# Optimization experiments

Measured on AMD Instinct MI355X. Metric: run time of the kernel, lower is better.

Reference implementation:

```python
import jax, jax.numpy as jnp
import numpy as np

N_NODES = 100000
N_EDGES = 3200000
N_GRAPHS = 1024

def _lin(x, W, b):
    return x @ W.T + b

def _gine(x, src, dst, edge_attr, W, b, n_nodes):
    # message = relu(x_j + e); aggregate sum at dst; out = Linear(x + aggr)  (eps=0)
    msg = jax.nn.relu(x[src] + edge_attr)
    aggr = jax.ops.segment_sum(msg, dst, num_segments=n_nodes)
    return _lin(x + aggr, W, b)

def setup_inputs() -> dict:
    key = jax.random.key(0)
    ks = jax.random.split(key, 20)
    D_NODE, D_EDGE, H, OUT = 12, 4, 15, 2
    inp = {
        "x": jax.random.normal(ks[0], (N_NODES, D_NODE), dtype=jnp.float32),
        "edge_index": jax.random.randint(ks[1], (2, N_EDGES), 0, N_NODES, dtype=jnp.int64),
        "edge_attr": jax.random.normal(ks[2], (N_EDGES, D_EDGE), dtype=jnp.float32),
        "batch": jnp.sort(jax.random.randint(ks[3], (N_NODES,), 0, N_GRAPHS, dtype=jnp.int64)),
        # edge converters
        "Wec1": jax.random.normal(ks[4], (D_NODE, D_EDGE), dtype=jnp.float32) * 0.3,
        "bec1": jnp.zeros((D_NODE,), jnp.float32),
        "Wec2": jax.random.normal(ks[5], (H, D_NODE), dtype=jnp.float32) * 0.2,
        "bec2": jnp.zeros((H,), jnp.float32),
        # GINE layer linears
        "Wl0": jax.random.normal(ks[6], (H, D_NODE), dtype=jnp.float32) * 0.2,
        "bl0": jnp.zeros((H,), jnp.float32),
        "Wl1": jax.random.normal(ks[7], (H, H), dtype=jnp.float32) * 0.2,
        "bl1": jnp.zeros((H,), jnp.float32),
        "Wl2": jax.random.normal(ks[8], (H, H), dtype=jnp.float32) * 0.2,
        "bl2": jnp.zeros((H,), jnp.float32),
        # output head
        "Wo1": jax.random.normal(ks[9], (H, H), dtype=jnp.float32) * 0.2,
        "bo1": jnp.zeros((H,), jnp.float32),
        "Wo2": jax.random.normal(ks[10], (OUT, H), dtype=jnp.float32) * 0.2,
        "bo2": jnp.zeros((OUT,), jnp.float32),
    }
    return inp

def reference(x, edge_index, edge_attr, batch,
              Wec1, bec1, Wec2, bec2,
              Wl0, bl0, Wl1, bl1, Wl2, bl2,
              Wo1, bo1, Wo2, bo2):
    src, dst = edge_index[0], edge_index[1]
    n = x.shape[0]
    ea = _lin(edge_attr, Wec1, bec1)                 # [E, 12]
    h = jax.nn.elu(_gine(x, src, dst, ea, Wl0, bl0, n))   # [N, 15]
    ea2 = _lin(ea, Wec2, bec2)                       # [E, 15]
    h = jax.nn.elu(_gine(h, src, dst, ea2, Wl1, bl1, n))
    h = jax.nn.elu(_gine(h, src, dst, ea2, Wl2, bl2, n))
    pooled = jax.ops.segment_sum(h, batch, num_segments=N_GRAPHS)  # [G, 15]
    out = _lin(pooled, Wo1, bo1)
    # dropout(p=0.1) is identity in eval mode
    out = _lin(out, Wo2, bo2)                        # [G, 2]
    return out
```

## Files before the change

kernel.cpp:

```cpp
#include <hip/hip_runtime.h>
#include <hip/hip_fp16.h>
#include <math.h>

#define D_NODE 12
#define HS     16
#define BSH    7
#define BSZ    128
#define CHUNK  8192
#define HALF   4096
#define MAXNB  1024

__device__ __forceinline__ int wave_iscan(int v, int lane) {
#pragma unroll
    for (int d = 1; d < 64; d <<= 1) {
        int u = __shfl_up(v, d, 64);
        if (lane >= d) v += u;
    }
    return v;
}

__device__ __forceinline__ uint2 pack4(float4 a) {
    __half2 lo = __floats2half2_rn(a.x, a.y);
    __half2 hi = __floats2half2_rn(a.z, a.w);
    uint2 r;
    r.x = *reinterpret_cast<unsigned*>(&lo);
    r.y = *reinterpret_cast<unsigned*>(&hi);
    return r;
}

__device__ __forceinline__ float4 unpack4(uint2 u) {
    __half2 lo = *reinterpret_cast<__half2*>(&u.x);
    __half2 hi = *reinterpret_cast<__half2*>(&u.y);
    float2 f0 = __half22float2(lo), f1 = __half22float2(hi);
    return make_float4(f0.x, f0.y, f1.x, f1.y);
}

__global__ __launch_bounds__(256) void k_xcvt(
    const float* __restrict__ x, long long nn, __half* __restrict__ xp)
{
    long long idx = (long long)blockIdx.x * 256 + threadIdx.x;
    if (idx >= nn * HS) return;
    long long n = idx >> 4;
    int l = (int)(idx & 15);
    xp[idx] = __float2half_rn((l < D_NODE) ? x[n * D_NODE + l] : 0.f);
}

__global__ __launch_bounds__(1024) void k_p1(
    const int* __restrict__ ei, long long ne, int NB, int* __restrict__ M)
{
    __shared__ int cnt[MAXNB];
    int t = threadIdx.x;
    for (int k = t; k < NB; k += 1024) cnt[k] = 0;
    __syncthreads();
    long long beg = (long long)blockIdx.x * CHUNK;
    long long end = beg + CHUNK; if (end > ne) end = ne;
    for (long long e = beg + t; e < end; e += 1024)
        atomicAdd(&cnt[ei[ne + e] >> BSH], 1);
    __syncthreads();
    int* row = M + (long long)blockIdx.x * NB;
    for (int k = t; k < NB; k += 1024) row[k] = cnt[k];
}

__global__ __launch_bounds__(256) void k_colscan(
    int* __restrict__ M, int nblk, int NB, int* __restrict__ tot)
{
    __shared__ int wsum[4];
    int k = blockIdx.x;
    int t = threadIdx.x;
    int lane = t & 63, wv = t >> 6;
    int v[4]; int s = 0;
#pragma unroll
    for (int j = 0; j < 4; ++j) {
        int b = t * 4 + j;
        v[j] = (b < nblk) ? M[(long long)b * NB + k] : 0;
        s += v[j];
    }
    int inc = wave_iscan(s, lane);
    if (lane == 63) wsum[wv] = inc;
    __syncthreads();
    int base = inc - s;
#pragma unroll
    for (int j = 0; j < 4; ++j) { if (j < wv) base += wsum[j]; }
#pragma unroll
    for (int j = 0; j < 4; ++j) {
        int b = t * 4 + j;
        if (b < nblk) { M[(long long)b * NB + k] = base; base += v[j]; }
    }
    if (t == 255) tot[k] = base;
}

__global__ __launch_bounds__(1024) void k_bb(
    const int* __restrict__ tot, int NB, int* __restrict__ bb)
{
    __shared__ int wsum[16];
    int t = threadIdx.x;
    int lane = t & 63, wv = t >> 6;
    int c = (t < NB) ? tot[t] : 0;
    int inc = wave_iscan(c, lane);
    if (lane == 63) wsum[wv] = inc;
    __syncthreads();
    if (t < 16) {
        int s2 = wsum[t];
#pragma unroll
        for (int d = 1; d < 16; d <<= 1) {
            int u = __shfl_up(s2, d, 64);
            if (t >= d) s2 += u;
        }
        wsum[t] = s2;
    }
    __syncthreads();
    int base = (wv == 0) ? 0 : wsum[wv - 1];
    int incl = base + inc;
    if (t < NB) bb[t] = incl - c;
    if (t == NB - 1) bb[NB] = incl;
}

__global__ __launch_bounds__(1024) void k_p2(
    const int* __restrict__ ei, long long ne, const float4* __restrict__ attr,
    const int* __restrict__ M, const int* __restrict__ bb, int NB,
    unsigned* __restrict__ sp1, uint2* __restrict__ sattr1)
{
    __shared__ int lcnt[MAXNB];
    __shared__ int excl[MAXNB];
    __shared__ int gb[MAXNB];
    __shared__ int wsum[16];
    __shared__ unsigned sp_st[HALF];
    __shared__ uint2   sat_st[HALF];
    __shared__ int     gd_st[HALF];
    int t = threadIdx.x;
    int lane = t & 63, wv = t >> 6;
    const int* row = M + (long long)blockIdx.x * NB;
    gb[t]   = (t < NB) ? (bb[t] + row[t]) : 0;
    lcnt[t] = 0;
    __syncthreads();
    long long beg = (long long)blockIdx.x * CHUNK;
    long long end = beg + CHUNK; if (end > ne) end = ne;
    int nloc = (int)(end - beg);
    unsigned pk8[8]; uint2 a8[8]; int k8[8], r8[8];
#pragma unroll
    for (int j = 0; j < 8; ++j) {
        long long e = beg + t + (long long)j * 1024;
        if (e < end) {
            int s = ei[e];
            int d = ei[ne + e];
            a8[j] = pack4(attr[e]);
            int k = d >> BSH;
            k8[j] = k;
            pk8[j] = (unsigned)s | ((unsigned)(d & (BSZ - 1)) << 20);
            r8[j] = atomicAdd(&lcnt[k], 1);
        } else k8[j] = -1;
    }
    __syncthreads();
    int c = lcnt[t];
    int inc = wave_iscan(c, lane);
    if (lane == 63) wsum[wv] = inc;
    __syncthreads();
    if (t < 16) {
        int s2 = wsum[t];
#pragma unroll
        for (int d = 1; d < 16; d <<= 1) {
            int u = __shfl_up(s2, d, 64);
            if (t >= d) s2 += u;
        }
        wsum[t] = s2;
    }
    __syncthreads();
    excl[t] = inc - c + ((wv == 0) ? 0 : wsum[wv - 1]);
    __syncthreads();
    int idx8[8];
#pragma unroll
    for (int j = 0; j < 8; ++j)
        idx8[j] = (k8[j] >= 0) ? (excl[k8[j]] + r8[j]) : -1;
#pragma unroll
    for (int q = 0; q < 2; ++q) {
        int lo = q * HALF;
#pragma unroll
        for (int j = 0; j < 8; ++j) {
            int idx = idx8[j] - lo;
            if (idx8[j] >= 0 && idx >= 0 && idx < HALF) {
                sp_st[idx]  = pk8[j];
                sat_st[idx] = a8[j];
                gd_st[idx]  = gb[k8[j]] + r8[j];
            }
        }
        __syncthreads();
        for (int p = t; p < HALF; p += 1024) {
            int gp = lo + p;
            if (gp < nloc) {
                int gd = gd_st[p];
                sp1[gd]    = sp_st[p];
                sattr1[gd] = sat_st[p];
            }
        }
        __syncthreads();
    }
}

__global__ __launch_bounds__(1024) void k_p3(
    const unsigned* __restrict__ sp1, const uint2* __restrict__ sattr1,
    const int* __restrict__ bb, int NB, long long nn,
    unsigned* __restrict__ sp2, uint2* __restrict__ sattr2, int* __restrict__ off)
{
    __shared__ int cnt[BSZ];
    __shared__ int stage[BSZ];
    __shared__ int wsum0;
    int k = blockIdx.x, t = threadIdx.x;
    int lane = t & 63, wv = t >> 6;
    int beg = bb[k], end = bb[k + 1];
    if (t < BSZ) cnt[t] = 0;
    __syncthreads();
    for (int e = beg + t; e < end; e += 1024)
        atomicAdd(&cnt[sp1[e] >> 20], 1);
    __syncthreads();
    if (t < BSZ) {
        int c = cnt[t];
        int inc = wave_iscan(c, lane);
        stage[t] = inc;
        if (lane == 63 && wv == 0) wsum0 = inc;
    }
    __syncthreads();
    if (t < BSZ) {
        int c = cnt[t];
        int incl = stage[t] + ((wv == 1) ? wsum0 : 0);
        int excl = beg + incl - c;
        long long n = (long long)k * BSZ + t;
        if (n < nn) off[n] = excl;
        cnt[t] = excl;
    }
    if (k == NB - 1 && t == 0) off[nn] = end;
    __syncthreads();
    for (int e = beg + t; e < end; e += 1024) {
        unsigned pk = sp1[e];
        int ld = pk >> 20;
        int p = atomicAdd(&cnt[ld], 1);
        sp2[p] = pk & 0xFFFFF;
        sattr2[p] = sattr1[e];
    }
}

__global__ __launch_bounds__(256) void k_layer0(
    const __half* __restrict__ xp, long long nn, const int* __restrict__ off,
    const unsigned* __restrict__ sp2, const uint2* __restrict__ sattr2,
    const float* __restrict__ Wec1, const float* __restrict__ bec1,
    const float* __restrict__ Wl, const float* __restrict__ bl,
    __half* __restrict__ hout)
{
    __shared__ float sW1[64], sb1[16], sWl[16 * 17], sbl[16];
    int t = threadIdx.x;
    if (t < 64)  sW1[t] = (t < 48) ? Wec1[t] : 0.f;
    if (t < 16)  sb1[t] = (t < 12) ? bec1[t] : 0.f;
    { int i = t >> 4, j = t & 15;
      sWl[i * 17 + j] = (i < 15 && j < 12) ? Wl[i * 12 + j] : 0.f; }
    if (t < 16)  sbl[t] = (t < 15) ? bl[t] : 0.f;
    __syncthreads();
    int g = t >> 4, l = t & 15;
    long long n = (long long)blockIdx.x * 16 + g;
    if (n >= nn) return;
    int beg = off[n], end = off[n + 1];
    float w0 = sW1[l*4+0], w1 = sW1[l*4+1], w2 = sW1[l*4+2], w3 = sW1[l*4+3];
    float b1 = sb1[l];
    float xn = __half2float(xp[(n << 4) + l]);
    float acc = 0.f;
#pragma unroll 8
    for (int e = beg; e < end; ++e) {
        unsigned s = sp2[e];
        float4 a = unpack4(sattr2[e]);
        float xs = __half2float(xp[((long long)s << 4) + l]);
        float ea = b1 + w0 * a.x + w1 * a.y + w2 * a.z + w3 * a.w;
        acc += fmaxf(xs + ea, 0.f);
    }
    float v = xn + acc;
    float r = sbl[l];
#pragma unroll
    for (int j = 0; j < 12; ++j) {
        float vj = __shfl(v, j, 16);
        r += vj * sWl[l * 17 + j];
    }
    float o = r > 0.f ? r : expm1f(r);
    hout[(n << 4) + l] = __float2half_rn((l < 15) ? o : 0.f);
}

template<bool POOL, bool STORE>
__global__ __launch_bounds__(256) void k_layerK(
    const __half* __restrict__ h, long long nn, const int* __restrict__ off,
    const unsigned* __restrict__ sp2, const uint2* __restrict__ sattr2,
    const float* __restrict__ Wec1, const float* __restrict__ bec1,
    const float* __restrict__ Wec2, const float* __restrict__ bec2,
    const float* __restrict__ Wl, const float* __restrict__ bl,
    __half* __restrict__ hout, const int* __restrict__ batch, float* __restrict__ pooled)
{
    __shared__ float sW12[64], sb12[16], sWl[16 * 17], sbl[16];
    int t = threadIdx.x;
    if (t < 64) {
        int i = t >> 2, kk = t & 3;
        float a = 0.f;
        if (i < 15) {
#pragma unroll
            for (int j = 0; j < 12; ++j) a += Wec2[i*12+j] * Wec1[j*4+kk];
        }
        sW12[t] = a;
    }
    if (t < 16) {
        float a = 0.f;
        if (t < 15) {
            a = bec2[t];
#pragma unroll
            for (int j = 0; j < 12; ++j) a += Wec2[t*12+j] * bec1[j];
        }
        sb12[t] = a;
    }
    { int i = t >> 4, j = t & 15;
      sWl[i * 17 + j] = (i < 15 && j < 15) ? Wl[i * 15 + j] : 0.f; }
    if (t < 16) sbl[t] = (t < 15) ? bl[t] : 0.f;
    __syncthreads();
    int g = t >> 4, l = t & 15;
    long long n = (long long)blockIdx.x * 16 + g;
    if (n >= nn) return;
    int beg = off[n], end = off[n + 1];
    float w0 = sW12[l*4+0], w1 = sW12[l*4+1], w2 = sW12[l*4+2], w3 = sW12[l*4+3];
    float b12 = sb12[l];
    float hn = __half2float(h[(n << 4) + l]);
    float acc = 0.f;
#pragma unroll 8
    for (int e = beg; e < end; ++e) {
        unsigned s = sp2[e];
        float4 a = unpack4(sattr2[e]);
        float hs = __half2float(h[((long long)s << 4) + l]);
        float e2 = b12 + w0 * a.x + w1 * a.y + w2 * a.z + w3 * a.w;
        acc += fmaxf(hs + e2, 0.f);
    }
    float v = hn + acc;
    float r = sbl[l];
#pragma unroll
    for (int j = 0; j < 15; ++j) {
        float vj = __shfl(v, j, 16);
        r += vj * sWl[l * 17 + j];
    }
    float o = r > 0.f ? r : expm1f(r);
    if (STORE) hout[(n << 4) + l] = __float2half_rn((l < 15) ? o : 0.f);
    if (POOL && l < 15) atomicAdd(&pooled[(long long)batch[n] * HS + l], o);
}

__global__ __launch_bounds__(256) void k_head(
    const float* __restrict__ pooled, long long ng,
    const float* __restrict__ Wo1, const float* __restrict__ bo1,
    const float* __restrict__ Wo2, const float* __restrict__ bo2,
    float* __restrict__ out)
{
    long long g = (long long)blockIdx.x * 256 + threadIdx.x;
    if (g >= ng) return;
    float p[15], m[15];
#pragma unroll
    for (int j = 0; j < 15; ++j) p[j] = pooled[g * HS + j];
#pragma unroll
    for (int i = 0; i < 15; ++i) {
        float acc = bo1[i];
#pragma unroll
        for (int j = 0; j < 15; ++j) acc += p[j] * Wo1[i * 15 + j];
        m[i] = acc;
    }
#pragma unroll
    for (int i = 0; i < 2; ++i) {
        float acc = bo2[i];
#pragma unroll
        for (int j = 0; j < 15; ++j) acc += m[j] * Wo2[i * 15 + j];
        out[g * 2 + i] = acc;
    }
}

extern "C" void kernel_launch(void* const* d_in, const int* in_sizes, int n_in,
                              void* d_out, int out_size, void* d_ws, size_t ws_size,
                              hipStream_t stream)
{
    const float* x    = (const float*)d_in[0];
    const int*   ei   = (const int*)d_in[1];
    const float* attr = (const float*)d_in[2];
    const int*   batch= (const int*)d_in[3];
    const float* Wec1 = (const float*)d_in[4];
    const float* bec1 = (const float*)d_in[5];
    const float* Wec2 = (const float*)d_in[6];
    const float* bec2 = (const float*)d_in[7];
    const float* Wl0  = (const float*)d_in[8];
    const float* bl0  = (const float*)d_in[9];
    const float* Wl1  = (const float*)d_in[10];
    const float* bl1  = (const float*)d_in[11];
    const float* Wl2  = (const float*)d_in[12];
    const float* bl2  = (const float*)d_in[13];
    const float* Wo1  = (const float*)d_in[14];
    const float* bo1  = (const float*)d_in[15];
    const float* Wo2  = (const float*)d_in[16];
    const float* bo2  = (const float*)d_in[17];

    const long long nn = in_sizes[0] / D_NODE;
    const long long ne = in_sizes[1] / 2;
    const long long ng = out_size / 2;

    const int NB   = (int)((nn + BSZ - 1) >> BSH);
    const int nblk = (int)((ne + CHUNK - 1) / CHUNK);

    char* w = (char*)d_ws;
    uint2*    sattr1 = (uint2*)w;                 w += (size_t)ne * sizeof(uint2);
    unsigned* sp1    = (unsigned*)w;              w += (size_t)ne * sizeof(unsigned);
    uint2*    sattr2 = (uint2*)w;                 w += (size_t)ne * sizeof(uint2);
    unsigned* sp2    = (unsigned*)w;              w += (size_t)ne * sizeof(unsigned);
    int*      M      = (int*)w;                   w += (size_t)nblk * NB * sizeof(int);
    int*      tot    = (int*)w;                   w += (size_t)NB * sizeof(int);
    int*      bb     = (int*)w;                   w += ((size_t)NB + 1) * sizeof(int);
    int*      off    = (int*)w;                   w += ((size_t)nn + 1) * sizeof(int);
    w = (char*)(((uintptr_t)w + 15) & ~(uintptr_t)15);
    __half*   xp     = (__half*)w;                w += (size_t)nn * HS * sizeof(__half);
    __half*   hA     = (__half*)sattr1;
    __half*   hB     = hA + (size_t)nn * HS;
    float*    pooled = (float*)(hB + (size_t)nn * HS);
    float*    out    = (float*)d_out;

    k_xcvt<<<(int)((nn * HS + 255) / 256), 256, 0, stream>>>(x, nn, xp);

    k_p1<<<nblk, 1024, 0, stream>>>(ei, ne, NB, M);
    k_colscan<<<NB, 256, 0, stream>>>(M, nblk, NB, tot);
    k_bb<<<1, 1024, 0, stream>>>(tot, NB, bb);
    k_p2<<<nblk, 1024, 0, stream>>>(ei, ne, (const float4*)attr, M, bb, NB, sp1, sattr1);
    k_p3<<<NB, 1024, 0, stream>>>(sp1, sattr1, bb, NB, nn, sp2, sattr2, off);

    const int lblk = (int)((nn + 15) / 16);
    k_layer0<<<lblk, 256, 0, stream>>>(xp, nn, off, sp2, sattr2, Wec1, bec1, Wl0, bl0, hA);
    k_layerK<false, true><<<lblk, 256, 0, stream>>>(hA, nn, off, sp2, sattr2,
        Wec1, bec1, Wec2, bec2, Wl1, bl1, hB, nullptr, nullptr);
    hipMemsetAsync(pooled, 0, (size_t)ng * HS * sizeof(float), stream);
    k_layerK<true, false><<<lblk, 256, 0, stream>>>(hB, nn, off, sp2, sattr2,
        Wec1, bec1, Wec2, bec2, Wl2, bl2, nullptr, batch, pooled);

    k_head<<<(int)((ng + 255) / 256), 256, 0, stream>>>(pooled, ng, Wo1, bo1, Wo2, bo2, out);
}
```

Baseline: 264.2 us.

## Split each node's edge loop across four 16-lane slots per wavefront

The GINE layer kernels now give each node a whole 64-lane wavefront instead of a 16-lane group. The four 16-lane slots process interleaved edges and combine their partial sums with xor shuffles. The goal is more memory-level parallelism per node and shorter serial gather loops, in exchange for four times more blocks and idle lanes on low-degree nodes. Edge arrays are padded so reads past the end stay in bounds, and source indices are masked to 20 bits.

Measured after the change: 324.8 us. 1.23x slower.

```diff
diff --git a/kernel.cpp b/kernel.cpp
--- a/kernel.cpp
+++ b/kernel.cpp
@@ -28,9 +28,9 @@
     return r;
 }
 
-__device__ __forceinline__ float4 unpack4(uint2 u) {
-    __half2 lo = *reinterpret_cast<__half2*>(&u.x);
-    __half2 hi = *reinterpret_cast<__half2*>(&u.y);
+__device__ __forceinline__ float4 unpack4(unsigned ux, unsigned uy) {
+    __half2 lo = *reinterpret_cast<__half2*>(&ux);
+    __half2 hi = *reinterpret_cast<__half2*>(&uy);
     float2 f0 = __half22float2(lo), f1 = __half22float2(hi);
     return make_float4(f0.x, f0.y, f1.x, f1.y);
 }
@@ -253,22 +253,30 @@
       sWl[i * 17 + j] = (i < 15 && j < 12) ? Wl[i * 12 + j] : 0.f; }
     if (t < 16)  sbl[t] = (t < 15) ? bl[t] : 0.f;
     __syncthreads();
-    int g = t >> 4, l = t & 15;
-    long long n = (long long)blockIdx.x * 16 + g;
+    int wv = t >> 6;
+    int lane = t & 63;
+    int l = lane & 15;
+    int slot = lane >> 4;
+    long long n = (long long)blockIdx.x * 4 + wv;
     if (n >= nn) return;
     int beg = off[n], end = off[n + 1];
     float w0 = sW1[l*4+0], w1 = sW1[l*4+1], w2 = sW1[l*4+2], w3 = sW1[l*4+3];
     float b1 = sb1[l];
     float xn = __half2float(xp[(n << 4) + l]);
     float acc = 0.f;
-#pragma unroll 8
-    for (int e = beg; e < end; ++e) {
-        unsigned s = sp2[e];
-        float4 a = unpack4(sattr2[e]);
-        float xs = __half2float(xp[((long long)s << 4) + l]);
+#pragma unroll 2
+    for (int e0 = beg; e0 < end; e0 += 4) {
+        int e = e0 + slot;
+        unsigned sp = sp2[e] & 0xFFFFF;
+        uint2 at = sattr2[e];
+        float4 a = unpack4(at.x, at.y);
+        float xs = __half2float(xp[((long long)sp << 4) + l]);
         float ea = b1 + w0 * a.x + w1 * a.y + w2 * a.z + w3 * a.w;
-        acc += fmaxf(xs + ea, 0.f);
-    }
+        float m = fmaxf(xs + ea, 0.f);
+        acc += (e < end) ? m : 0.f;
+    }
+    acc += __shfl_xor(acc, 16, 64);
+    acc += __shfl_xor(acc, 32, 64);
     float v = xn + acc;
     float r = sbl[l];
 #pragma unroll
@@ -277,7 +285,8 @@
         r += vj * sWl[l * 17 + j];
     }
     float o = r > 0.f ? r : expm1f(r);
-    hout[(n << 4) + l] = __float2half_rn((l < 15) ? o : 0.f);
+    if (slot == 0)
+        hout[(n << 4) + l] = __float2half_rn((l < 15) ? o : 0.f);
 }
 
 template<bool POOL, bool STORE>
@@ -313,22 +322,30 @@
       sWl[i * 17 + j] = (i < 15 && j < 15) ? Wl[i * 15 + j] : 0.f; }
     if (t < 16) sbl[t] = (t < 15) ? bl[t] : 0.f;
     __syncthreads();
-    int g = t >> 4, l = t & 15;
-    long long n = (long long)blockIdx.x * 16 + g;
+    int wv = t >> 6;
+    int lane = t & 63;
+    int l = lane & 15;
+    int slot = lane >> 4;
+    long long n = (long long)blockIdx.x * 4 + wv;
     if (n >= nn) return;
     int beg = off[n], end = off[n + 1];
     float w0 = sW12[l*4+0], w1 = sW12[l*4+1], w2 = sW12[l*4+2], w3 = sW12[l*4+3];
     float b12 = sb12[l];
     float hn = __half2float(h[(n << 4) + l]);
     float acc = 0.f;
-#pragma unroll 8
-    for (int e = beg; e < end; ++e) {
-        unsigned s = sp2[e];
-        float4 a = unpack4(sattr2[e]);
-        float hs = __half2float(h[((long long)s << 4) + l]);
+#pragma unroll 2
+    for (int e0 = beg; e0 < end; e0 += 4) {
+        int e = e0 + slot;
+        unsigned sp = sp2[e] & 0xFFFFF;
+        uint2 at = sattr2[e];
+        float4 a = unpack4(at.x, at.y);
+        float hs = __half2float(h[((long long)sp << 4) + l]);
         float e2 = b12 + w0 * a.x + w1 * a.y + w2 * a.z + w3 * a.w;
-        acc += fmaxf(hs + e2, 0.f);
-    }
+        float m = fmaxf(hs + e2, 0.f);
+        acc += (e < end) ? m : 0.f;
+    }
+    acc += __shfl_xor(acc, 16, 64);
+    acc += __shfl_xor(acc, 32, 64);
     float v = hn + acc;
     float r = sbl[l];
 #pragma unroll
@@ -337,8 +354,10 @@
         r += vj * sWl[l * 17 + j];
     }
     float o = r > 0.f ? r : expm1f(r);
-    if (STORE) hout[(n << 4) + l] = __float2half_rn((l < 15) ? o : 0.f);
-    if (POOL && l < 15) atomicAdd(&pooled[(long long)batch[n] * HS + l], o);
+    if (slot == 0) {
+        if (STORE) hout[(n << 4) + l] = __float2half_rn((l < 15) ? o : 0.f);
+        if (POOL && l < 15) atomicAdd(&pooled[(long long)batch[n] * HS + l], o);
+    }
 }
 
 __global__ __launch_bounds__(256) void k_head(
@@ -397,12 +416,13 @@
 
     const int NB   = (int)((nn + BSZ - 1) >> BSH);
     const int nblk = (int)((ne + CHUNK - 1) / CHUNK);
+    const long long nep = ne + 8;
 
     char* w = (char*)d_ws;
-    uint2*    sattr1 = (uint2*)w;                 w += (size_t)ne * sizeof(uint2);
-    unsigned* sp1    = (unsigned*)w;              w += (size_t)ne * sizeof(unsigned);
-    uint2*    sattr2 = (uint2*)w;                 w += (size_t)ne * sizeof(uint2);
-    unsigned* sp2    = (unsigned*)w;              w += (size_t)ne * sizeof(unsigned);
+    uint2*    sattr1 = (uint2*)w;                 w += (size_t)nep * sizeof(uint2);
+    unsigned* sp1    = (unsigned*)w;              w += (size_t)nep * sizeof(unsigned);
+    uint2*    sattr2 = (uint2*)w;                 w += (size_t)nep * sizeof(uint2);
+    unsigned* sp2    = (unsigned*)w;              w += (size_t)nep * sizeof(unsigned);
     int*      M      = (int*)w;                   w += (size_t)nblk * NB * sizeof(int);
     int*      tot    = (int*)w;                   w += (size_t)NB * sizeof(int);
     int*      bb     = (int*)w;                   w += ((size_t)NB + 1) * sizeof(int);
@@ -422,7 +442,7 @@
     k_p2<<<nblk, 1024, 0, stream>>>(ei, ne, (const float4*)attr, M, bb, NB, sp1, sattr1);
     k_p3<<<NB, 1024, 0, stream>>>(sp1, sattr1, bb, NB, nn, sp2, sattr2, off);
 
-    const int lblk = (int)((nn + 15) / 16);
+    const int lblk = (int)((nn + 3) / 4);
     k_layer0<<<lblk, 256, 0, stream>>>(xp, nn, off, sp2, sattr2, Wec1, bec1, Wl0, bl0, hA);
     k_layerK<false, true><<<lblk, 256, 0, stream>>>(hA, nn, off, sp2, sattr2,
         Wec1, bec1, Wec2, bec2, Wl1, bl1, hB, nullptr, nullptr);
```
